# Optimization experiments

Hardware: AMD Instinct MI355X
Metric: run time of the kernel (lower is better)

The kernel has to match this reference:

```python
import jax, jax.numpy as jnp
import numpy as np


def _cal_similarity(query, respond):
    # query: [B, n1, d], respond: [B, n2, d]
    # scores[b, c, q, r] = <query[b, q], respond[c, r]>
    scores = jnp.einsum('bqd,crd->bcqr', query, respond)  # [B, B, n1, n2]
    # max over respond tokens, mean over query tokens -> [B, B]
    return scores.max(axis=-1).mean(axis=-1)


def _ce_with_arange_labels(logits):
    # cross-entropy with labels = arange(B), mean reduction
    logp = jax.nn.log_softmax(logits, axis=-1)
    return -jnp.mean(jnp.diagonal(logp))


def setup_inputs() -> dict:
    key = jax.random.key(0)
    k1, k2 = jax.random.split(key)
    B, n1, n2, d = 96, 196, 77, 512
    image_out = jax.random.normal(k1, (B, n1, d), dtype=jnp.float32)
    text_out = jax.random.normal(k2, (B, n2, d), dtype=jnp.float32)
    return {"image_out": image_out, "text_out": text_out}


def reference(image_out, text_out):
    i2t = _cal_similarity(image_out, text_out)  # [B, B]
    t2i = _cal_similarity(text_out, image_out)  # [B, B]
    return 0.5 * (_ce_with_arange_labels(i2t) + _ce_with_arange_labels(t2i))
```

## Files before the change

kernel.cpp:

```cpp
#include <hip/hip_runtime.h>
#include <math.h>

#define BB 96
#define N1 196
#define N2 77
#define DD 512

#define IMGN (BB * N1 * DD)
#define TXTN (BB * N2 * DD)

#define ATILES 13
#define NTILES 24
#define BUFH (NTILES * 512)

#define TA_TILES (BB * 13 * 16)
#define TB_TILES (BB * 5 * 16)
#define NT_TILES (TA_TILES + TB_TILES)

#define NSTRIPS_A (BB * 13)
#define NSTRIPS_B (BB * 5)
#define NSTRIPS   (NSTRIPS_A + NSTRIPS_B)

typedef _Float16 f16x8 __attribute__((ext_vector_type(8)));
typedef float f4v __attribute__((ext_vector_type(4)));

typedef unsigned int __attribute__((address_space(1))) as1_uint;
typedef unsigned int __attribute__((address_space(3))) as3_uint;

__device__ __forceinline__ void gload_lds16(const void* g, void* l) {
    __builtin_amdgcn_global_load_lds((const as1_uint*)g, (as3_uint*)l, 16, 0, 0);
}

__global__ __launch_bounds__(256) void convert_tiled_kernel(
    const float* __restrict__ img, const float* __restrict__ txt,
    _Float16* __restrict__ dst)
{
    __shared__ _Float16 sh[16 * 520];
    const int sid = blockIdx.x;
    const int tid = threadIdx.x;
    const float* base;
    int rowbase, rmax, tile0;
    if (sid < NSTRIPS_A) {
        const int bi = sid / 13, s = sid % 13;
        base = img + (size_t)bi * N1 * DD;
        rowbase = s * 16; rmax = N1 - 1;
        tile0 = sid * 16;
    } else {
        const int bs = sid - NSTRIPS_A;
        const int bt = bs / 5, ct = bs % 5;
        base = txt + (size_t)bt * N2 * DD;
        rowbase = ct * 16; rmax = N2 - 1;
        tile0 = TA_TILES + bs * 16;
    }
#pragma unroll
    for (int it = 0; it < 8; ++it) {
        const int u  = it * 256 + tid;
        const int r  = u >> 7;
        const int c4 = u & 127;
        int q = rowbase + r; q = q > rmax ? rmax : q;
        float4 v = *(const float4*)(base + (size_t)q * DD + c4 * 4);
        union { _Float16 h[4]; uint2 u2; } o;
        o.h[0] = (_Float16)v.x; o.h[1] = (_Float16)v.y;
        o.h[2] = (_Float16)v.z; o.h[3] = (_Float16)v.w;
        *(uint2*)(sh + r * 520 + c4 * 4) = o.u2;
    }
    __syncthreads();
#pragma unroll
    for (int it = 0; it < 4; ++it) {
        const int w  = it * 256 + tid;
        const int kc = w >> 6;
        const int c  = w & 63;
        const int r16 = c & 15, k8 = c >> 4;
        uint4 val = *(const uint4*)(sh + r16 * 520 + kc * 32 + k8 * 8);
        *(uint4*)(dst + (size_t)(tile0 + kc) * 512 + c * 8) = val;
    }
}

template <int SG0, int NS, int H>
__device__ __forceinline__ void compute_sub(const f16x8* __restrict__ fr,
                                            f4v* __restrict__ acc, int lane) {
    f16x8 b[5];
#pragma unroll
    for (int ct = 0; ct < 5; ++ct)
        b[ct] = fr[(ATILES + H * 5 + ct) * 64 + lane];
#pragma unroll
    for (int i = 0; i < NS; ++i) {
        f16x8 a = fr[(SG0 + i) * 64 + lane];
#pragma unroll
        for (int ct = 0; ct < 5; ++ct)
            acc[i * 5 + ct] = __builtin_amdgcn_mfma_f32_16x16x32_f16(
                a, b[ct], acc[i * 5 + ct], 0, 0, 0);
    }
}

template <int SG0, int NS, int H>
__device__ __forceinline__ void reduce_phase1(const f4v* __restrict__ acc,
                                              int g, int lq, int lm,
                                              float* __restrict__ rp,
                                              float* __restrict__ cp) {
    float colm[5];
#pragma unroll
    for (int ct = 0; ct < 5; ++ct) colm[ct] = -INFINITY;
#pragma unroll
    for (int i = 0; i < NS; ++i) {
        const int s = SG0 + i;
        float rowm[4] = {-INFINITY, -INFINITY, -INFINITY, -INFINITY};
        bool rows_ok = (s != 12) || (lq == 0);
#pragma unroll
        for (int ct = 0; ct < 5; ++ct) {
            f4v a = acc[i * 5 + ct];
            bool col_ok = (ct != 4) || (lm < N2 - 64);
            float cm = fmaxf(fmaxf(a[0], a[1]), fmaxf(a[2], a[3]));
            colm[ct] = fmaxf(colm[ct], rows_ok ? cm : -INFINITY);
#pragma unroll
            for (int r = 0; r < 4; ++r)
                rowm[r] = fmaxf(rowm[r], col_ok ? a[r] : -INFINITY);
        }
#pragma unroll
        for (int r = 0; r < 4; ++r) {
            float m = rowm[r];
            m = fmaxf(m, __shfl_xor(m, 1));
            m = fmaxf(m, __shfl_xor(m, 2));
            m = fmaxf(m, __shfl_xor(m, 4));
            m = fmaxf(m, __shfl_xor(m, 8));
            if (lm == 0) rp[H * 208 + s * 16 + lq * 4 + r] = m;
        }
    }
#pragma unroll
    for (int ct = 0; ct < 5; ++ct) {
        float m = colm[ct];
        m = fmaxf(m, __shfl_xor(m, 16));
        m = fmaxf(m, __shfl_xor(m, 32));
        if (lq == 0) cp[g * 160 + H * 80 + ct * 16 + lm] = m;
    }
}

template <bool PRE>
__global__ __launch_bounds__(256, 2) void sim_mfma_kernel(
    const float* __restrict__ imgF, const float* __restrict__ txtF,
    const _Float16* __restrict__ h16,
    float* __restrict__ i2t, float* __restrict__ t2i)
{
    const int id  = blockIdx.x;
    const int xcd = id & 7;
    const int lid = id >> 3;
    const int w   = lid % 48;
    const int btq = lid / 48;
    const int btp = btq * 4 + (w & 3);
    const int bi  = xcd * 12 + (w >> 2);
    const int bt0 = btp * 2;

    const int tid = threadIdx.x;
    const int wave = tid >> 6, lane = tid & 63;
    const int lm = lane & 15;
    const int lq = lane >> 4;
    const int g = wave >> 1;

    __shared__ __align__(16) _Float16 lds[3 * BUFH];
    float* scratch = (float*)(lds + 2 * BUFH);
    float* rp   = scratch;
    float* cp   = scratch + 416;
    float* sws  = scratch + 736;
    float* scol = scratch + 740;

    int off[6];
    const float* fsrc[6];
#pragma unroll
    for (int j = 0; j < 6; ++j) {
        const int T = 4 * j + wave;
        if constexpr (PRE) {
            int t;
            if (T < ATILES) {
                t = (bi * 13 + T) * 16;
            } else if (T < 23) {
                const int ct = T - ATILES;
                const int bt = bt0 + (ct >= 5);
                t = TA_TILES + (bt * 5 + (ct % 5)) * 16;
            } else {
                t = 0;
            }
            off[j] = t * 512 + lane * 8;
        } else {
            int o;
            bool isA = true;
            if (T < ATILES) {
                int q = T * 16 + lm; q = q > (N1 - 1) ? (N1 - 1) : q;
                o = (bi * N1 + q) * DD + lq * 8;
            } else if (T < 23) {
                isA = false;
                int ct = T - ATILES;
                int bt = bt0 + (ct >= 5);
                int r = (ct % 5) * 16 + lm; r = r > (N2 - 1) ? (N2 - 1) : r;
                o = (bt * N2 + r) * DD + lq * 8;
            } else {
                o = lq * 8;
            }
            off[j] = o;
            fsrc[j] = isA ? imgF : txtF;
        }
    }

    auto stage = [&](int kc, int b) {
        const int k0 = kc * 512;
#pragma unroll
        for (int j = 0; j < 6; ++j)
            gload_lds16(h16 + off[j] + k0,
                        lds + (b * NTILES + 4 * j + wave) * 512);
    };

    f4v acc[35];
#pragma unroll
    for (int i = 0; i < 35; ++i) acc[i] = (f4v){0.f, 0.f, 0.f, 0.f};

    auto do_compute = [&](const f16x8* fr) {
        if (wave == 0)      compute_sub<0, 7, 0>(fr, acc, lane);
        else if (wave == 1) compute_sub<0, 7, 1>(fr, acc, lane);
        else if (wave == 2) compute_sub<7, 6, 0>(fr, acc, lane);
        else                compute_sub<7, 6, 1>(fr, acc, lane);
    };

    if constexpr (PRE) {
        stage(0, 0);
        stage(1, 1);
#pragma unroll 1
        for (int kc = 0; kc < 16; ++kc) {
            if (kc < 14) {
                stage(kc + 2, (kc + 2) % 3);
                asm volatile("s_waitcnt vmcnt(12)" ::: "memory");
            } else if (kc == 14) {
                asm volatile("s_waitcnt vmcnt(6)" ::: "memory");
            } else {
                asm volatile("s_waitcnt vmcnt(0)" ::: "memory");
            }
            __builtin_amdgcn_s_barrier();
            asm volatile("" ::: "memory");
            do_compute((const f16x8*)(lds + (kc % 3) * BUFH));
            asm volatile("" ::: "memory");
            __builtin_amdgcn_s_barrier();
        }
    } else {
#pragma unroll 1
        for (int kc = 0; kc < 16; ++kc) {
            __syncthreads();
            const int k0 = kc * 32;
#pragma unroll
            for (int j = 0; j < 6; ++j) {
                const int T = 4 * j + wave;
                if (T < 23) {
                    float4 v0 = *(const float4*)(fsrc[j] + off[j] + k0);
                    float4 v1 = *(const float4*)(fsrc[j] + off[j] + k0 + 4);
                    union { f16x8 f; uint4 u; } o;
                    o.f[0] = (_Float16)v0.x; o.f[1] = (_Float16)v0.y;
                    o.f[2] = (_Float16)v0.z; o.f[3] = (_Float16)v0.w;
                    o.f[4] = (_Float16)v1.x; o.f[5] = (_Float16)v1.y;
                    o.f[6] = (_Float16)v1.z; o.f[7] = (_Float16)v1.w;
                    ((uint4*)lds)[T * 64 + lane] = o.u;
                }
            }
            __syncthreads();
            do_compute((const f16x8*)lds);
        }
        __syncthreads();
    }

    if (wave == 0)      reduce_phase1<0, 7, 0>(acc, g, lq, lm, rp, cp);
    else if (wave == 1) reduce_phase1<0, 7, 1>(acc, g, lq, lm, rp, cp);
    else if (wave == 2) reduce_phase1<7, 6, 0>(acc, g, lq, lm, rp, cp);
    else                reduce_phase1<7, 6, 1>(acc, g, lq, lm, rp, cp);
    __syncthreads();

    {
        const int h = wave & 1;
        const int sseg = wave >> 1;
        const int qa = sseg * 128 + lane;
        const int qb = qa + 64;
        float v = rp[h * 208 + qa];
        if (qb < N1) v += rp[h * 208 + qb];
        v += __shfl_xor(v, 1);  v += __shfl_xor(v, 2);  v += __shfl_xor(v, 4);
        v += __shfl_xor(v, 8);  v += __shfl_xor(v, 16); v += __shfl_xor(v, 32);
        if (lane == 0) sws[wave] = v;
    }
    if (tid < 160) scol[tid] = fmaxf(cp[tid], cp[160 + tid]);
    __syncthreads();
    if (tid == 0)
        i2t[bi * BB + bt0] = (sws[0] + sws[2]) * (1.f / (float)N1);
    if (tid == 1)
        i2t[bi * BB + bt0 + 1] = (sws[1] + sws[3]) * (1.f / (float)N1);
    if (wave < 2) {
        const float* c = scol + wave * 80;
        float cv = c[lane] + ((lane < N2 - 64) ? c[64 + lane] : 0.f);
        cv += __shfl_xor(cv, 1);  cv += __shfl_xor(cv, 2);  cv += __shfl_xor(cv, 4);
        cv += __shfl_xor(cv, 8);  cv += __shfl_xor(cv, 16); cv += __shfl_xor(cv, 32);
        if (lane == 0)
            t2i[(bt0 + wave) * BB + bi] = cv * (1.f / (float)N2);
    }
}

__global__ __launch_bounds__(256) void ce_kernel(
    const float* __restrict__ i2t, const float* __restrict__ t2i,
    float* __restrict__ out)
{
    const int tid = threadIdx.x;
    const int wid = tid >> 6;
    const int lane = tid & 63;

    float contrib = 0.f;
    if (tid < 2 * BB) {
        const float* M = (tid < BB) ? i2t : t2i;
        const int b = (tid < BB) ? tid : tid - BB;
        const float* row = M + b * BB;
        float mx = row[0];
#pragma unroll 1
        for (int c = 1; c < BB; ++c) mx = fmaxf(mx, row[c]);
        float s = 0.f;
#pragma unroll 1
        for (int c = 0; c < BB; ++c) s += expf(row[c] - mx);
        float lse = mx + logf(s);
        contrib = row[b] - lse;
    }
    contrib += __shfl_xor(contrib, 1);
    contrib += __shfl_xor(contrib, 2);
    contrib += __shfl_xor(contrib, 4);
    contrib += __shfl_xor(contrib, 8);
    contrib += __shfl_xor(contrib, 16);
    contrib += __shfl_xor(contrib, 32);

    __shared__ float s_part[4];
    if (lane == 0) s_part[wid] = contrib;
    __syncthreads();
    if (tid == 0) {
        float total = s_part[0] + s_part[1] + s_part[2] + s_part[3];
        out[0] = -total * (1.f / (float)(2 * BB));
    }
}

extern "C" void kernel_launch(void* const* d_in, const int* in_sizes, int n_in,
                              void* d_out, int out_size, void* d_ws, size_t ws_size,
                              hipStream_t stream) {
    const float* img = (const float*)d_in[0];
    const float* txt = (const float*)d_in[1];
    float* i2t = (float*)d_ws;
    float* t2i = i2t + BB * BB;

    const size_t conv_off = 2 * BB * BB * sizeof(float);
    const size_t need = conv_off + (size_t)NT_TILES * 512 * sizeof(_Float16);

    const int nblocks = BB * (BB / 2);
    if (ws_size >= need) {
        _Float16* h16 = (_Float16*)((char*)d_ws + conv_off);
        convert_tiled_kernel<<<NSTRIPS, 256, 0, stream>>>(img, txt, h16);
        sim_mfma_kernel<true><<<nblocks, 256, 0, stream>>>(img, txt, h16, i2t, t2i);
    } else {
        sim_mfma_kernel<false><<<nblocks, 256, 0, stream>>>(img, txt, nullptr, i2t, t2i);
    }
    ce_kernel<<<1, 256, 0, stream>>>(i2t, t2i, (float*)d_out);
}
```

Baseline: 309.4 us.

## Widen block to 16 waves covering four text items per image tile

Each block now computes one image against four text items instead of two, using 1024 threads (16 waves) that split the image row tiles four ways and the text column groups four ways. This doubles reuse of each staged image tile, halves the block count and shrinks per-wave accumulators from 35 to 20 MFMA tiles, which reduces register pressure. The LDS buffer grows to 33 tiles per stage with triple buffering, and wait counts are adjusted per wave for the uneven load split. The reduction scratch is moved to the start of LDS, and per-wave reductions write results directly. Risks include lower occupancy from the larger LDS footprint and higher barrier cost with 16 waves.

```diff
diff --git a/kernel.cpp b/kernel.cpp
--- a/kernel.cpp
+++ b/kernel.cpp
@@ -10,7 +10,8 @@
 #define TXTN (BB * N2 * DD)
 
 #define ATILES 13
-#define NTILES 24
+#define BTILES 20
+#define NTILES 33
 #define BUFH (NTILES * 512)
 
 #define TA_TILES (BB * 13 * 16)
@@ -76,13 +77,13 @@
     }
 }
 
-template <int SG0, int NS, int H>
+template <int SG0, int NS, int CG>
 __device__ __forceinline__ void compute_sub(const f16x8* __restrict__ fr,
                                             f4v* __restrict__ acc, int lane) {
     f16x8 b[5];
 #pragma unroll
     for (int ct = 0; ct < 5; ++ct)
-        b[ct] = fr[(ATILES + H * 5 + ct) * 64 + lane];
+        b[ct] = fr[(ATILES + CG * 5 + ct) * 64 + lane];
 #pragma unroll
     for (int i = 0; i < NS; ++i) {
         f16x8 a = fr[(SG0 + i) * 64 + lane];
@@ -93,7 +94,7 @@
     }
 }
 
-template <int SG0, int NS, int H>
+template <int SG0, int NS, int CG>
 __device__ __forceinline__ void reduce_phase1(const f4v* __restrict__ acc,
                                               int g, int lq, int lm,
                                               float* __restrict__ rp,
@@ -123,7 +124,7 @@
             m = fmaxf(m, __shfl_xor(m, 2));
             m = fmaxf(m, __shfl_xor(m, 4));
             m = fmaxf(m, __shfl_xor(m, 8));
-            if (lm == 0) rp[H * 208 + s * 16 + lq * 4 + r] = m;
+            if (lm == 0) rp[CG * 208 + s * 16 + lq * 4 + r] = m;
         }
     }
 #pragma unroll
@@ -131,12 +132,12 @@
         float m = colm[ct];
         m = fmaxf(m, __shfl_xor(m, 16));
         m = fmaxf(m, __shfl_xor(m, 32));
-        if (lq == 0) cp[g * 160 + H * 80 + ct * 16 + lm] = m;
+        if (lq == 0) cp[g * 320 + CG * 80 + ct * 16 + lm] = m;
     }
 }
 
 template <bool PRE>
-__global__ __launch_bounds__(256, 2) void sim_mfma_kernel(
+__global__ __launch_bounds__(1024, 4) void sim_mfma_kernel(
     const float* __restrict__ imgF, const float* __restrict__ txtF,
     const _Float16* __restrict__ h16,
     float* __restrict__ i2t, float* __restrict__ t2i)
@@ -144,56 +145,51 @@
     const int id  = blockIdx.x;
     const int xcd = id & 7;
     const int lid = id >> 3;
-    const int w   = lid % 48;
-    const int btq = lid / 48;
-    const int btp = btq * 4 + (w & 3);
-    const int bi  = xcd * 12 + (w >> 2);
-    const int bt0 = btp * 2;
+    const int bi  = xcd * 12 + lid / 24;
+    const int btq = lid % 24;
+    const int bt0 = btq * 4;
 
     const int tid = threadIdx.x;
     const int wave = tid >> 6, lane = tid & 63;
     const int lm = lane & 15;
     const int lq = lane >> 4;
-    const int g = wave >> 1;
+    const int g  = wave >> 2;
 
     __shared__ __align__(16) _Float16 lds[3 * BUFH];
-    float* scratch = (float*)(lds + 2 * BUFH);
+    float* scratch = (float*)lds;
     float* rp   = scratch;
-    float* cp   = scratch + 416;
-    float* sws  = scratch + 736;
-    float* scol = scratch + 740;
-
-    int off[6];
-    const float* fsrc[6];
-#pragma unroll
-    for (int j = 0; j < 6; ++j) {
-        const int T = 4 * j + wave;
+    float* cp   = scratch + 832;
+    float* scol = scratch + 2112;
+
+    int off[3];
+    const float* fsrc[3];
+#pragma unroll
+    for (int j = 0; j < 3; ++j) {
+        const int T = 16 * j + wave;
         if constexpr (PRE) {
-            int t;
+            int t = 0;
             if (T < ATILES) {
                 t = (bi * 13 + T) * 16;
-            } else if (T < 23) {
-                const int ct = T - ATILES;
-                const int bt = bt0 + (ct >= 5);
-                t = TA_TILES + (bt * 5 + (ct % 5)) * 16;
-            } else {
-                t = 0;
+            } else if (T < NTILES) {
+                const int jj = T - ATILES;
+                const int cgj = jj / 5, ct = jj % 5;
+                const int bt = bt0 + cgj;
+                t = TA_TILES + (bt * 5 + ct) * 16;
             }
             off[j] = t * 512 + lane * 8;
         } else {
-            int o;
+            int o = 0;
             bool isA = true;
             if (T < ATILES) {
                 int q = T * 16 + lm; q = q > (N1 - 1) ? (N1 - 1) : q;
                 o = (bi * N1 + q) * DD + lq * 8;
-            } else if (T < 23) {
+            } else if (T < NTILES) {
                 isA = false;
-                int ct = T - ATILES;
-                int bt = bt0 + (ct >= 5);
-                int r = (ct % 5) * 16 + lm; r = r > (N2 - 1) ? (N2 - 1) : r;
+                const int jj = T - ATILES;
+                const int cgj = jj / 5, ct = jj % 5;
+                const int bt = bt0 + cgj;
+                int r = ct * 16 + lm; r = r > (N2 - 1) ? (N2 - 1) : r;
                 o = (bt * N2 + r) * DD + lq * 8;
-            } else {
-                o = lq * 8;
             }
             off[j] = o;
             fsrc[j] = isA ? imgF : txtF;
@@ -203,20 +199,33 @@
     auto stage = [&](int kc, int b) {
         const int k0 = kc * 512;
 #pragma unroll
-        for (int j = 0; j < 6; ++j)
-            gload_lds16(h16 + off[j] + k0,
-                        lds + (b * NTILES + 4 * j + wave) * 512);
+        for (int j = 0; j < 3; ++j)
+            if (16 * j + wave < NTILES)
+                gload_lds16(h16 + off[j] + k0,
+                            lds + (b * NTILES + 16 * j + wave) * 512);
     };
 
-    f4v acc[35];
-#pragma unroll
-    for (int i = 0; i < 35; ++i) acc[i] = (f4v){0.f, 0.f, 0.f, 0.f};
+    f4v acc[20];
+#pragma unroll
+    for (int i = 0; i < 20; ++i) acc[i] = (f4v){0.f, 0.f, 0.f, 0.f};
 
     auto do_compute = [&](const f16x8* fr) {
-        if (wave == 0)      compute_sub<0, 7, 0>(fr, acc, lane);
-        else if (wave == 1) compute_sub<0, 7, 1>(fr, acc, lane);
-        else if (wave == 2) compute_sub<7, 6, 0>(fr, acc, lane);
-        else                compute_sub<7, 6, 1>(fr, acc, lane);
+        if      (wave ==  0) compute_sub<0, 4, 0>(fr, acc, lane);
+        else if (wave ==  1) compute_sub<0, 4, 1>(fr, acc, lane);
+        else if (wave ==  2) compute_sub<0, 4, 2>(fr, acc, lane);
+        else if (wave ==  3) compute_sub<0, 4, 3>(fr, acc, lane);
+        else if (wave ==  4) compute_sub<4, 3, 0>(fr, acc, lane);
+        else if (wave ==  5) compute_sub<4, 3, 1>(fr, acc, lane);
+        else if (wave ==  6) compute_sub<4, 3, 2>(fr, acc, lane);
+        else if (wave ==  7) compute_sub<4, 3, 3>(fr, acc, lane);
+        else if (wave ==  8) compute_sub<7, 3, 0>(fr, acc, lane);
+        else if (wave ==  9) compute_sub<7, 3, 1>(fr, acc, lane);
+        else if (wave == 10) compute_sub<7, 3, 2>(fr, acc, lane);
+        else if (wave == 11) compute_sub<7, 3, 3>(fr, acc, lane);
+        else if (wave == 12) compute_sub<10, 3, 0>(fr, acc, lane);
+        else if (wave == 13) compute_sub<10, 3, 1>(fr, acc, lane);
+        else if (wave == 14) compute_sub<10, 3, 2>(fr, acc, lane);
+        else                 compute_sub<10, 3, 3>(fr, acc, lane);
     };
 
     if constexpr (PRE) {
@@ -226,9 +235,11 @@
         for (int kc = 0; kc < 16; ++kc) {
             if (kc < 14) {
                 stage(kc + 2, (kc + 2) % 3);
-                asm volatile("s_waitcnt vmcnt(12)" ::: "memory");
+                if (wave == 0) asm volatile("s_waitcnt vmcnt(6)" ::: "memory");
+                else           asm volatile("s_waitcnt vmcnt(4)" ::: "memory");
             } else if (kc == 14) {
-                asm volatile("s_waitcnt vmcnt(6)" ::: "memory");
+                if (wave == 0) asm volatile("s_waitcnt vmcnt(3)" ::: "memory");
+                else           asm volatile("s_waitcnt vmcnt(2)" ::: "memory");
             } else {
                 asm volatile("s_waitcnt vmcnt(0)" ::: "memory");
             }
@@ -244,9 +255,9 @@
             __syncthreads();
             const int k0 = kc * 32;
 #pragma unroll
-            for (int j = 0; j < 6; ++j) {
-                const int T = 4 * j + wave;
-                if (T < 23) {
+            for (int j = 0; j < 3; ++j) {
+                const int T = 16 * j + wave;
+                if (T < NTILES) {
                     float4 v0 = *(const float4*)(fsrc[j] + off[j] + k0);
                     float4 v1 = *(const float4*)(fsrc[j] + off[j] + k0 + 4);
                     union { f16x8 f; uint4 u; } o;
@@ -263,36 +274,44 @@
         __syncthreads();
     }
 
-    if (wave == 0)      reduce_phase1<0, 7, 0>(acc, g, lq, lm, rp, cp);
-    else if (wave == 1) reduce_phase1<0, 7, 1>(acc, g, lq, lm, rp, cp);
-    else if (wave == 2) reduce_phase1<7, 6, 0>(acc, g, lq, lm, rp, cp);
-    else                reduce_phase1<7, 6, 1>(acc, g, lq, lm, rp, cp);
+    if      (wave ==  0) reduce_phase1<0, 4, 0>(acc, g, lq, lm, rp, cp);
+    else if (wave ==  1) reduce_phase1<0, 4, 1>(acc, g, lq, lm, rp, cp);
+    else if (wave ==  2) reduce_phase1<0, 4, 2>(acc, g, lq, lm, rp, cp);
+    else if (wave ==  3) reduce_phase1<0, 4, 3>(acc, g, lq, lm, rp, cp);
+    else if (wave ==  4) reduce_phase1<4, 3, 0>(acc, g, lq, lm, rp, cp);
+    else if (wave ==  5) reduce_phase1<4, 3, 1>(acc, g, lq, lm, rp, cp);
+    else if (wave ==  6) reduce_phase1<4, 3, 2>(acc, g, lq, lm, rp, cp);
+    else if (wave ==  7) reduce_phase1<4, 3, 3>(acc, g, lq, lm, rp, cp);
+    else if (wave ==  8) reduce_phase1<7, 3, 0>(acc, g, lq, lm, rp, cp);
+    else if (wave ==  9) reduce_phase1<7, 3, 1>(acc, g, lq, lm, rp, cp);
+    else if (wave == 10) reduce_phase1<7, 3, 2>(acc, g, lq, lm, rp, cp);
+    else if (wave == 11) reduce_phase1<7, 3, 3>(acc, g, lq, lm, rp, cp);
+    else if (wave == 12) reduce_phase1<10, 3, 0>(acc, g, lq, lm, rp, cp);
+    else if (wave == 13) reduce_phase1<10, 3, 1>(acc, g, lq, lm, rp, cp);
+    else if (wave == 14) reduce_phase1<10, 3, 2>(acc, g, lq, lm, rp, cp);
+    else                 reduce_phase1<10, 3, 3>(acc, g, lq, lm, rp, cp);
     __syncthreads();
 
-    {
-        const int h = wave & 1;
-        const int sseg = wave >> 1;
-        const int qa = sseg * 128 + lane;
-        const int qb = qa + 64;
-        float v = rp[h * 208 + qa];
-        if (qb < N1) v += rp[h * 208 + qb];
+    if (wave < 4) {
+        const float* r = rp + wave * 208;
+        float v = r[lane] + r[64 + lane] + r[128 + lane]
+                + ((lane < 4) ? r[192 + lane] : 0.f);
         v += __shfl_xor(v, 1);  v += __shfl_xor(v, 2);  v += __shfl_xor(v, 4);
         v += __shfl_xor(v, 8);  v += __shfl_xor(v, 16); v += __shfl_xor(v, 32);
-        if (lane == 0) sws[wave] = v;
-    }
-    if (tid < 160) scol[tid] = fmaxf(cp[tid], cp[160 + tid]);
+        if (lane == 0) i2t[bi * BB + bt0 + wave] = v * (1.f / (float)N1);
+    }
+    if (tid < 320)
+        scol[tid] = fmaxf(fmaxf(cp[tid], cp[320 + tid]),
+                          fmaxf(cp[640 + tid], cp[960 + tid]));
     __syncthreads();
-    if (tid == 0)
-        i2t[bi * BB + bt0] = (sws[0] + sws[2]) * (1.f / (float)N1);
-    if (tid == 1)
-        i2t[bi * BB + bt0 + 1] = (sws[1] + sws[3]) * (1.f / (float)N1);
-    if (wave < 2) {
-        const float* c = scol + wave * 80;
+    if (wave >= 4 && wave < 8) {
+        const int c4 = wave - 4;
+        const float* c = scol + c4 * 80;
         float cv = c[lane] + ((lane < N2 - 64) ? c[64 + lane] : 0.f);
         cv += __shfl_xor(cv, 1);  cv += __shfl_xor(cv, 2);  cv += __shfl_xor(cv, 4);
         cv += __shfl_xor(cv, 8);  cv += __shfl_xor(cv, 16); cv += __shfl_xor(cv, 32);
         if (lane == 0)
-            t2i[(bt0 + wave) * BB + bi] = cv * (1.f / (float)N2);
+            t2i[(bt0 + c4) * BB + bi] = cv * (1.f / (float)N2);
     }
 }
 
@@ -345,13 +364,13 @@
     const size_t conv_off = 2 * BB * BB * sizeof(float);
     const size_t need = conv_off + (size_t)NT_TILES * 512 * sizeof(_Float16);
 
-    const int nblocks = BB * (BB / 2);
+    const int nblocks = BB * (BB / 4);
     if (ws_size >= need) {
         _Float16* h16 = (_Float16*)((char*)d_ws + conv_off);
         convert_tiled_kernel<<<NSTRIPS, 256, 0, stream>>>(img, txt, h16);
-        sim_mfma_kernel<true><<<nblocks, 256, 0, stream>>>(img, txt, h16, i2t, t2i);
+        sim_mfma_kernel<true><<<nblocks, 1024, 0, stream>>>(img, txt, h16, i2t, t2i);
     } else {
-        sim_mfma_kernel<false><<<nblocks, 256, 0, stream>>>(img, txt, nullptr, i2t, t2i);
+        sim_mfma_kernel<false><<<nblocks, 1024, 0, stream>>>(img, txt, nullptr, i2t, t2i);
     }
     ce_kernel<<<1, 256, 0, stream>>>(i2t, t2i, (float*)d_out);
 }
```

Measured after the change: 303.9 us. About the same (-1.8%).

## Split similarity block across eight waves with B fragments loaded directly from global

Applied to the files above, without the earlier changes.

Each similarity block now runs 512 threads, with eight waves each computing a smaller slice of the image tiles. Only the image tiles are staged through LDS. Text B fragments are read straight from global memory into registers each k-step, which cuts LDS footprint and accumulator count per wave and is meant to raise occupancy and latency hiding. The final cross-entropy kernel is also rewritten to handle one row per wave with shuffle reductions instead of serial loops per thread. The risk is extra global traffic for the duplicated B loads and wait counts that must match the new per-wave load counts.

```diff
diff --git a/kernel.cpp b/kernel.cpp
--- a/kernel.cpp
+++ b/kernel.cpp
@@ -10,7 +10,7 @@
 #define TXTN (BB * N2 * DD)
 
 #define ATILES 13
-#define NTILES 24
+#define NTILES 13
 #define BUFH (NTILES * 512)
 
 #define TA_TILES (BB * 13 * 16)
@@ -76,13 +76,10 @@
     }
 }
 
-template <int SG0, int NS, int H>
+template <int SG0, int NS>
 __device__ __forceinline__ void compute_sub(const f16x8* __restrict__ fr,
+                                            const f16x8* __restrict__ b,
                                             f4v* __restrict__ acc, int lane) {
-    f16x8 b[5];
-#pragma unroll
-    for (int ct = 0; ct < 5; ++ct)
-        b[ct] = fr[(ATILES + H * 5 + ct) * 64 + lane];
 #pragma unroll
     for (int i = 0; i < NS; ++i) {
         f16x8 a = fr[(SG0 + i) * 64 + lane];
@@ -136,7 +133,7 @@
 }
 
 template <bool PRE>
-__global__ __launch_bounds__(256, 2) void sim_mfma_kernel(
+__global__ __launch_bounds__(512, 4) void sim_mfma_kernel(
     const float* __restrict__ imgF, const float* __restrict__ txtF,
     const _Float16* __restrict__ h16,
     float* __restrict__ i2t, float* __restrict__ t2i)
@@ -155,68 +152,48 @@
     const int lm = lane & 15;
     const int lq = lane >> 4;
     const int g = wave >> 1;
+    const int h = wave & 1;
 
     __shared__ __align__(16) _Float16 lds[3 * BUFH];
-    float* scratch = (float*)(lds + 2 * BUFH);
-    float* rp   = scratch;
-    float* cp   = scratch + 416;
-    float* sws  = scratch + 736;
-    float* scol = scratch + 740;
-
-    int off[6];
-    const float* fsrc[6];
-#pragma unroll
-    for (int j = 0; j < 6; ++j) {
-        const int T = 4 * j + wave;
-        if constexpr (PRE) {
-            int t;
-            if (T < ATILES) {
-                t = (bi * 13 + T) * 16;
-            } else if (T < 23) {
-                const int ct = T - ATILES;
-                const int bt = bt0 + (ct >= 5);
-                t = TA_TILES + (bt * 5 + (ct % 5)) * 16;
-            } else {
-                t = 0;
-            }
-            off[j] = t * 512 + lane * 8;
-        } else {
-            int o;
-            bool isA = true;
-            if (T < ATILES) {
-                int q = T * 16 + lm; q = q > (N1 - 1) ? (N1 - 1) : q;
-                o = (bi * N1 + q) * DD + lq * 8;
-            } else if (T < 23) {
-                isA = false;
-                int ct = T - ATILES;
-                int bt = bt0 + (ct >= 5);
-                int r = (ct % 5) * 16 + lm; r = r > (N2 - 1) ? (N2 - 1) : r;
-                o = (bt * N2 + r) * DD + lq * 8;
-            } else {
-                o = lq * 8;
-            }
-            off[j] = o;
-            fsrc[j] = isA ? imgF : txtF;
-        }
-    }
+    float* rp   = (float*)lds;
+    float* cp   = (float*)lds + 416;
+    float* sws  = (float*)lds + 1056;
+    float* scol = (float*)lds + 1064;
+
+    int offA0 = 0, offA1 = 0;
+    const float* fA0; const float* fA1;
+    if constexpr (PRE) {
+        offA0 = ((bi * 13 + wave) * 16) * 512 + lane * 8;
+        if (wave < 5) offA1 = ((bi * 13 + 8 + wave) * 16) * 512 + lane * 8;
+    } else {
+        int q0 = wave * 16 + lm; q0 = q0 > (N1 - 1) ? (N1 - 1) : q0;
+        offA0 = (bi * N1 + q0) * DD + lq * 8;
+        fA0 = imgF;
+        int q1 = (8 + wave) * 16 + lm; q1 = q1 > (N1 - 1) ? (N1 - 1) : q1;
+        offA1 = (bi * N1 + q1) * DD + lq * 8;
+        fA1 = imgF;
+    }
+
+    const f16x8* gb = nullptr;
+    if constexpr (PRE)
+        gb = (const f16x8*)h16 + (TA_TILES + (bt0 + h) * 5 * 16) * 64 + lane;
 
     auto stage = [&](int kc, int b) {
         const int k0 = kc * 512;
-#pragma unroll
-        for (int j = 0; j < 6; ++j)
-            gload_lds16(h16 + off[j] + k0,
-                        lds + (b * NTILES + 4 * j + wave) * 512);
+        gload_lds16(h16 + offA0 + k0, lds + (b * NTILES + wave) * 512);
+        if (wave < 5)
+            gload_lds16(h16 + offA1 + k0, lds + (b * NTILES + 8 + wave) * 512);
     };
 
-    f4v acc[35];
-#pragma unroll
-    for (int i = 0; i < 35; ++i) acc[i] = (f4v){0.f, 0.f, 0.f, 0.f};
-
-    auto do_compute = [&](const f16x8* fr) {
-        if (wave == 0)      compute_sub<0, 7, 0>(fr, acc, lane);
-        else if (wave == 1) compute_sub<0, 7, 1>(fr, acc, lane);
-        else if (wave == 2) compute_sub<7, 6, 0>(fr, acc, lane);
-        else                compute_sub<7, 6, 1>(fr, acc, lane);
+    f4v acc[20];
+#pragma unroll
+    for (int i = 0; i < 20; ++i) acc[i] = (f4v){0.f, 0.f, 0.f, 0.f};
+
+    auto do_compute = [&](const f16x8* fr, const f16x8* b) {
+        if (wave == 0 || wave == 1)      compute_sub<0, 4>(fr, b, acc, lane);
+        else if (wave == 2 || wave == 3) compute_sub<4, 3>(fr, b, acc, lane);
+        else if (wave == 4 || wave == 5) compute_sub<7, 3>(fr, b, acc, lane);
+        else                             compute_sub<10, 3>(fr, b, acc, lane);
     };
 
     if constexpr (PRE) {
@@ -224,31 +201,32 @@
         stage(1, 1);
 #pragma unroll 1
         for (int kc = 0; kc < 16; ++kc) {
-            if (kc < 14) {
-                stage(kc + 2, (kc + 2) % 3);
-                asm volatile("s_waitcnt vmcnt(12)" ::: "memory");
-            } else if (kc == 14) {
-                asm volatile("s_waitcnt vmcnt(6)" ::: "memory");
-            } else {
-                asm volatile("s_waitcnt vmcnt(0)" ::: "memory");
-            }
+            f16x8 bfr[5];
+#pragma unroll
+            for (int ct = 0; ct < 5; ++ct)
+                bfr[ct] = gb[ct * 1024 + kc * 64];
+            if (kc + 2 < 16) stage(kc + 2, (kc + 2) % 3);
+            if (wave < 5) asm volatile("s_waitcnt vmcnt(9)" ::: "memory");
+            else          asm volatile("s_waitcnt vmcnt(7)" ::: "memory");
             __builtin_amdgcn_s_barrier();
             asm volatile("" ::: "memory");
-            do_compute((const f16x8*)(lds + (kc % 3) * BUFH));
+            do_compute((const f16x8*)(lds + (kc % 3) * BUFH), bfr);
             asm volatile("" ::: "memory");
             __builtin_amdgcn_s_barrier();
         }
     } else {
+        const int btf = bt0 + h;
 #pragma unroll 1
         for (int kc = 0; kc < 16; ++kc) {
             __syncthreads();
             const int k0 = kc * 32;
 #pragma unroll
-            for (int j = 0; j < 6; ++j) {
-                const int T = 4 * j + wave;
-                if (T < 23) {
-                    float4 v0 = *(const float4*)(fsrc[j] + off[j] + k0);
-                    float4 v1 = *(const float4*)(fsrc[j] + off[j] + k0 + 4);
+            for (int j = 0; j < 2; ++j) {
+                const int T = j * 8 + wave;
+                if (j == 0 || wave < 5) {
+                    const float* src = (j ? fA1 : fA0) + (j ? offA1 : offA0) + k0;
+                    float4 v0 = *(const float4*)(src);
+                    float4 v1 = *(const float4*)(src + 4);
                     union { f16x8 f; uint4 u; } o;
                     o.f[0] = (_Float16)v0.x; o.f[1] = (_Float16)v0.y;
                     o.f[2] = (_Float16)v0.z; o.f[3] = (_Float16)v0.w;
@@ -258,34 +236,55 @@
                 }
             }
             __syncthreads();
-            do_compute((const f16x8*)lds);
+            f16x8 bfr[5];
+#pragma unroll
+            for (int ct = 0; ct < 5; ++ct) {
+                int r = ct * 16 + lm; r = r > (N2 - 1) ? (N2 - 1) : r;
+                const float* src = txtF + (btf * N2 + r) * DD + k0 + lq * 8;
+                float4 v0 = *(const float4*)(src);
+                float4 v1 = *(const float4*)(src + 4);
+                f16x8 f;
+                f[0] = (_Float16)v0.x; f[1] = (_Float16)v0.y;
+                f[2] = (_Float16)v0.z; f[3] = (_Float16)v0.w;
+                f[4] = (_Float16)v1.x; f[5] = (_Float16)v1.y;
+                f[6] = (_Float16)v1.z; f[7] = (_Float16)v1.w;
+                bfr[ct] = f;
+            }
+            do_compute((const f16x8*)lds, bfr);
         }
         __syncthreads();
     }
 
-    if (wave == 0)      reduce_phase1<0, 7, 0>(acc, g, lq, lm, rp, cp);
-    else if (wave == 1) reduce_phase1<0, 7, 1>(acc, g, lq, lm, rp, cp);
-    else if (wave == 2) reduce_phase1<7, 6, 0>(acc, g, lq, lm, rp, cp);
-    else                reduce_phase1<7, 6, 1>(acc, g, lq, lm, rp, cp);
+    if (wave == 0)      reduce_phase1<0, 4, 0>(acc, g, lq, lm, rp, cp);
+    else if (wave == 1) reduce_phase1<0, 4, 1>(acc, g, lq, lm, rp, cp);
+    else if (wave == 2) reduce_phase1<4, 3, 0>(acc, g, lq, lm, rp, cp);
+    else if (wave == 3) reduce_phase1<4, 3, 1>(acc, g, lq, lm, rp, cp);
+    else if (wave == 4) reduce_phase1<7, 3, 0>(acc, g, lq, lm, rp, cp);
+    else if (wave == 5) reduce_phase1<7, 3, 1>(acc, g, lq, lm, rp, cp);
+    else if (wave == 6) reduce_phase1<10, 3, 0>(acc, g, lq, lm, rp, cp);
+    else                reduce_phase1<10, 3, 1>(acc, g, lq, lm, rp, cp);
     __syncthreads();
 
     {
-        const int h = wave & 1;
-        const int sseg = wave >> 1;
-        const int qa = sseg * 128 + lane;
-        const int qb = qa + 64;
-        float v = rp[h * 208 + qa];
-        if (qb < N1) v += rp[h * 208 + qb];
+        const int half = tid >> 8;
+        const int t = tid & 255;
+        float v = (t < N1) ? rp[half * 208 + t] : 0.f;
         v += __shfl_xor(v, 1);  v += __shfl_xor(v, 2);  v += __shfl_xor(v, 4);
         v += __shfl_xor(v, 8);  v += __shfl_xor(v, 16); v += __shfl_xor(v, 32);
         if (lane == 0) sws[wave] = v;
     }
-    if (tid < 160) scol[tid] = fmaxf(cp[tid], cp[160 + tid]);
+    if (tid < 160) {
+        float m = fmaxf(fmaxf(cp[tid], cp[160 + tid]),
+                        fmaxf(cp[320 + tid], cp[480 + tid]));
+        scol[tid] = m;
+    }
     __syncthreads();
     if (tid == 0)
-        i2t[bi * BB + bt0] = (sws[0] + sws[2]) * (1.f / (float)N1);
+        i2t[bi * BB + bt0] =
+            (sws[0] + sws[1] + sws[2] + sws[3]) * (1.f / (float)N1);
     if (tid == 1)
-        i2t[bi * BB + bt0 + 1] = (sws[1] + sws[3]) * (1.f / (float)N1);
+        i2t[bi * BB + bt0 + 1] =
+            (sws[4] + sws[5] + sws[6] + sws[7]) * (1.f / (float)N1);
     if (wave < 2) {
         const float* c = scol + wave * 80;
         float cv = c[lane] + ((lane < N2 - 64) ? c[64 + lane] : 0.f);
@@ -296,41 +295,40 @@
     }
 }
 
-__global__ __launch_bounds__(256) void ce_kernel(
+__global__ __launch_bounds__(1024) void ce_kernel(
     const float* __restrict__ i2t, const float* __restrict__ t2i,
     float* __restrict__ out)
 {
     const int tid = threadIdx.x;
-    const int wid = tid >> 6;
+    const int wave = tid >> 6;
     const int lane = tid & 63;
 
-    float contrib = 0.f;
-    if (tid < 2 * BB) {
-        const float* M = (tid < BB) ? i2t : t2i;
-        const int b = (tid < BB) ? tid : tid - BB;
-        const float* row = M + b * BB;
-        float mx = row[0];
+    float total = 0.f;
 #pragma unroll 1
-        for (int c = 1; c < BB; ++c) mx = fmaxf(mx, row[c]);
-        float s = 0.f;
-#pragma unroll 1
-        for (int c = 0; c < BB; ++c) s += expf(row[c] - mx);
-        float lse = mx + logf(s);
-        contrib = row[b] - lse;
-    }
-    contrib += __shfl_xor(contrib, 1);
-    contrib += __shfl_xor(contrib, 2);
-    contrib += __shfl_xor(contrib, 4);
-    contrib += __shfl_xor(contrib, 8);
-    contrib += __shfl_xor(contrib, 16);
-    contrib += __shfl_xor(contrib, 32);
-
-    __shared__ float s_part[4];
-    if (lane == 0) s_part[wid] = contrib;
+    for (int rr = 0; rr < 12; ++rr) {
+        const int row = rr * 16 + wave;
+        const float* M = (row < BB) ? i2t : t2i;
+        const int b = (row < BB) ? row : row - BB;
+        const float* r = M + b * BB;
+        float a = r[lane];
+        float c = (lane < BB - 64) ? r[64 + lane] : -INFINITY;
+        float m = fmaxf(a, c);
+        m = fmaxf(m, __shfl_xor(m, 1));  m = fmaxf(m, __shfl_xor(m, 2));
+        m = fmaxf(m, __shfl_xor(m, 4));  m = fmaxf(m, __shfl_xor(m, 8));
+        m = fmaxf(m, __shfl_xor(m, 16)); m = fmaxf(m, __shfl_xor(m, 32));
+        float s = expf(a - m) + ((lane < BB - 64) ? expf(c - m) : 0.f);
+        s += __shfl_xor(s, 1);  s += __shfl_xor(s, 2);  s += __shfl_xor(s, 4);
+        s += __shfl_xor(s, 8);  s += __shfl_xor(s, 16); s += __shfl_xor(s, 32);
+        total += r[b] - (m + logf(s));
+    }
+    __shared__ float sp[16];
+    if (lane == 0) sp[wave] = total;
     __syncthreads();
     if (tid == 0) {
-        float total = s_part[0] + s_part[1] + s_part[2] + s_part[3];
-        out[0] = -total * (1.f / (float)(2 * BB));
+        float t = 0.f;
+#pragma unroll
+        for (int i = 0; i < 16; ++i) t += sp[i];
+        out[0] = -t * (1.f / (float)(2 * BB));
     }
 }
 
@@ -349,9 +347,9 @@
     if (ws_size >= need) {
         _Float16* h16 = (_Float16*)((char*)d_ws + conv_off);
         convert_tiled_kernel<<<NSTRIPS, 256, 0, stream>>>(img, txt, h16);
-        sim_mfma_kernel<true><<<nblocks, 256, 0, stream>>>(img, txt, h16, i2t, t2i);
+        sim_mfma_kernel<true><<<nblocks, 512, 0, stream>>>(img, txt, h16, i2t, t2i);
     } else {
-        sim_mfma_kernel<false><<<nblocks, 256, 0, stream>>>(img, txt, nullptr, i2t, t2i);
-    }
-    ce_kernel<<<1, 256, 0, stream>>>(i2t, t2i, (float*)d_out);
-}
+        sim_mfma_kernel<false><<<nblocks, 512, 0, stream>>>(img, txt, nullptr, i2t, t2i);
+    }
+    ce_kernel<<<1, 1024, 0, stream>>>(i2t, t2i, (float*)d_out);
+}
```

After: 281.0 us. 1.1x faster.
